# Performance work log

Measured on AMD Instinct MI355X. Metric: run time of the kernel, lower is better.

Reference implementation:

```python
import jax, jax.numpy as jnp
import numpy as np

S, D, H, E = 4096, 1024, 16, 64  # seq_len, embed_dim, n_heads, head_size


def setup_inputs() -> dict:
    key = jax.random.key(0)
    ks = jax.random.split(key, 8)
    s_d = 1.0 / np.sqrt(D).astype(np.float32)
    return {
        "x": jax.random.normal(ks[0], (S, D), jnp.float32),
        # per-head Q/K/V projections (no bias), stacked over heads: [H, D, E]
        "Wk": jax.random.normal(ks[1], (H, D, E), jnp.float32) * s_d,
        "Wq": jax.random.normal(ks[2], (H, D, E), jnp.float32) * s_d,
        "Wv": jax.random.normal(ks[3], (H, D, E), jnp.float32) * s_d,
        # output projection Dense(D) with bias
        "Wo": jax.random.normal(ks[4], (H * E, D), jnp.float32) * (1.0 / np.sqrt(H * E).astype(np.float32)),
        "bo": jnp.zeros((D,), jnp.float32),
        # MLP: Dense(4D) -> gelu -> Dense(D), both with bias
        "W1": jax.random.normal(ks[5], (D, 4 * D), jnp.float32) * s_d,
        "b1": jnp.zeros((4 * D,), jnp.float32),
        "W2": jax.random.normal(ks[6], (4 * D, D), jnp.float32) * (1.0 / np.sqrt(4 * D).astype(np.float32)),
        "b2": jnp.zeros((D,), jnp.float32),
    }


def _attention(x, Wk, Wq, Wv):
    # per-head projections, vectorized over heads (original loops in Python)
    k = jnp.einsum('sd,hde->hse', x, Wk)
    q = jnp.einsum('sd,hde->hse', x, Wq)
    v = jnp.einsum('sd,hde->hse', x, Wv)
    # NOTE: original computes keys @ queries.T -> scores[i, j] = k_i . q_j
    scores = jnp.einsum('hse,hte->hst', k, q) / jnp.sqrt(jnp.float32(E))
    mask = jnp.tril(jnp.ones((x.shape[0], x.shape[0]), dtype=bool))  # [S, S]
    w = jax.nn.softmax(jnp.where(mask, scores, -jnp.inf), axis=-1)   # [H, S, S]
    out = jnp.einsum('hst,hte->hse', w, v)                            # [H, S, E]
    # concatenate heads along feature axis (head 0 first, matching the loop)
    return out.transpose(1, 0, 2).reshape(x.shape[0], -1)             # [S, H*E]


def reference(x, Wk, Wq, Wv, Wo, bo, W1, b1, W2, b2):
    x = x + _attention(x, Wk, Wq, Wv) @ Wo + bo
    h = jax.nn.gelu(x @ W1 + b1, approximate=True)  # flax default gelu (tanh approx)
    return x + h @ W2 + b2
```

## Files before the change

### kernel.cpp

```cpp
#include <hip/hip_runtime.h>

typedef __attribute__((ext_vector_type(8))) short s16x8;
typedef __attribute__((ext_vector_type(4))) short s16x4;
typedef __attribute__((ext_vector_type(4))) float f32x4;


__device__ __forceinline__ unsigned short f2bf(float f) {
    union { float f; unsigned u; } v; v.f = f;
    unsigned r = v.u + 0x7FFFu + ((v.u >> 16) & 1u);
    return (unsigned short)(r >> 16);
}

__device__ __forceinline__ float bf2f(unsigned short b) {
    union { unsigned u; float f; } v; v.u = ((unsigned)b) << 16;
    return v.f;
}

__device__ __forceinline__ unsigned cvt_pk_bf16(float lo, float hi) {
    unsigned r;
    asm("v_cvt_pk_bf16_f32 %0, %1, %2" : "=v"(r) : "v"(lo), "v"(hi));
    return r;
}

__device__ __forceinline__ float exp2_fast(float x) {
    float r;
    asm("v_exp_f32 %0, %1" : "=v"(r) : "v"(x));
    return r;
}

__device__ __forceinline__ float gelu_tanh(float x) {
    float u = 0.7978845608028654f * (x + 0.044715f * x * x * x);
    float au = fabsf(u);
    float t = 1.f - 2.f / (__expf(2.f * au) + 1.f);
    t = (u < 0.f) ? -t : t;
    return 0.5f * x * (1.f + t);
}

__device__ __forceinline__ void load_lds16(const void* g, void* l) {
    __builtin_amdgcn_global_load_lds(
        (const __attribute__((address_space(1))) void*)g,
        (__attribute__((address_space(3))) void*)l, 16, 0, 0);
}

__device__ __forceinline__ void xcd_remap(int& bx, int& by) {
    const int gx = gridDim.x;
    const int nwg = gx * gridDim.y;
    const int id = by * gx + bx;
    const int nid = (id & 7) * (nwg >> 3) + (id >> 3);
    bx = nid % gx; by = nid / gx;
}


__global__ void convert_bf16_k(const float* __restrict__ in,
                               unsigned short* __restrict__ out, int n) {
    int i = (blockIdx.x * blockDim.x + threadIdx.x) * 4;
    if (i >= n) return;
    float4 v = *(const float4*)(in + i);
    ushort4 o;
    o.x = f2bf(v.x); o.y = f2bf(v.y); o.z = f2bf(v.z); o.w = f2bf(v.w);
    *(ushort4*)(out + i) = o;
}

__global__ void transpose_k(const float* __restrict__ in,
                            unsigned short* __restrict__ out, int R, int C) {
    __shared__ float tile[32][33];
    const int b = blockIdx.z;
    const int c0 = blockIdx.x * 32, r0 = blockIdx.y * 32;
    const float* inb = in + (size_t)b * R * C;
    unsigned short* outb = out + (size_t)b * R * C;
    const int tx = threadIdx.x, ty = threadIdx.y;
    #pragma unroll
    for (int i = 0; i < 4; ++i)
        tile[ty + i*8][tx] = inb[(size_t)(r0 + ty + i*8) * C + c0 + tx];
    __syncthreads();
    #pragma unroll
    for (int i = 0; i < 4; ++i)
        outb[(size_t)(c0 + ty + i*8) * R + r0 + tx] = f2bf(tile[tx][ty + i*8]);
}

template<int EPI>
__global__ __launch_bounds__(256) void gemm_bt(
    const unsigned short* __restrict__ A,
    const unsigned short* __restrict__ BT,
    const float* __restrict__ bias,
    const float* __restrict__ resid,
    float* __restrict__ Cf,
    unsigned short* __restrict__ Cb,
    int M, int N, int K, int klen)
{
    __shared__ unsigned short As[3][128 * 32];
    __shared__ unsigned short Bs[3][128 * 32];
    const int tid = threadIdx.x;
    const int w  = tid >> 6, l = tid & 63;
    const int wr = w >> 1,  wc = w & 1;
    const int lg = l >> 4,  ll = l & 15;
    int bx = blockIdx.x, by = blockIdx.y;
    xcd_remap(bx, by);
    const int m0 = by * 128, n0 = bx * 128;
    const int koff = (EPI == 5) ? (int)blockIdx.z * klen : 0;

    const int srow = w * 16 + (l >> 2);
    const int scol = (((l & 3) ^ ((l >> 2) & 3))) * 8;

    f32x4 acc[4][4] = {};

    auto stage = [&](int buf, int k0) {
        #pragma unroll
        for (int i = 0; i < 2; ++i) {
            load_lds16(A  + (size_t)(m0 + srow + i*64) * K + koff + k0 + scol,
                       (char*)As[buf] + i*4096 + w*1024);
            load_lds16(BT + (size_t)(n0 + srow + i*64) * K + koff + k0 + scol,
                       (char*)Bs[buf] + i*4096 + w*1024);
        }
    };

    const int nsteps = ((EPI == 5) ? klen : K) >> 5;
    stage(0, 0); stage(1, 32);
    int buf = 0;
    for (int s = 0; s < nsteps; ++s) {
        if (s + 1 < nsteps) asm volatile("s_waitcnt vmcnt(4)" ::: "memory");
        else                asm volatile("s_waitcnt vmcnt(0)" ::: "memory");
        __builtin_amdgcn_s_barrier();
        s16x8 a[4], b[4];
        #pragma unroll
        for (int m = 0; m < 4; ++m) {
            const int row = wr*64 + m*16 + ll;
            a[m] = *(const s16x8*)&As[buf][row * 32 + ((lg ^ (ll & 3)) * 8)];
        }
        #pragma unroll
        for (int n = 0; n < 4; ++n) {
            const int row = wc*64 + n*16 + ll;
            b[n] = *(const s16x8*)&Bs[buf][row * 32 + ((lg ^ (ll & 3)) * 8)];
        }
        int bnext = buf + 2; if (bnext >= 3) bnext -= 3;
        if (s + 2 < nsteps) stage(bnext, (s + 2) << 5);
        __builtin_amdgcn_s_setprio(1);
        #pragma unroll
        for (int m = 0; m < 4; ++m)
            #pragma unroll
            for (int n = 0; n < 4; ++n)
                acc[m][n] = __builtin_amdgcn_mfma_f32_16x16x32_bf16(a[m], b[n], acc[m][n], 0, 0, 0);
        __builtin_amdgcn_s_setprio(0);
        buf = (buf == 2) ? 0 : buf + 1;
    }

    unsigned short* Cbz = (EPI == 5) ? (Cb + (size_t)blockIdx.z * M * N) : Cb;
    #pragma unroll
    for (int m = 0; m < 4; ++m) {
        #pragma unroll
        for (int n = 0; n < 4; ++n) {
            const int col = n0 + wc*64 + n*16 + ll;
            #pragma unroll
            for (int r = 0; r < 4; ++r) {
                const int row = m0 + wr*64 + m*16 + lg*4 + r;
                float v = acc[m][n][r];
                if constexpr (EPI == 2) v = gelu_tanh(v + bias[col]);
                if constexpr (EPI == 4) v *= (col < 1024) ? 0.1803368801f : 1.0f;
                Cbz[(size_t)row * N + col] = f2bf(v);
            }
        }
    }
}

__global__ __launch_bounds__(512) void gemm_mlp1_k(
    const unsigned short* __restrict__ A,
    const unsigned short* __restrict__ BT,
    const float* __restrict__ bias,
    unsigned short* __restrict__ Cb,
    int M, int N, int K)
{
    __shared__ unsigned short As[3][256 * 32];
    __shared__ unsigned short Bs[3][128 * 32];
    const int tid = threadIdx.x;
    const int w  = tid >> 6, l = tid & 63;
    const int wr = w >> 1,  wc = w & 1;
    const int lg = l >> 4,  ll = l & 15;
    int bx = blockIdx.x, by = blockIdx.y;
    xcd_remap(bx, by);
    const int m0 = by * 256, n0 = bx * 128;

    const int srowA = w * 16 + (l >> 2);
    const int scolA = (((l & 3) ^ ((l >> 2) & 3))) * 8;
    const int srowB = tid >> 2;
    const int scolB = (((tid & 3) ^ ((tid >> 2) & 3))) * 8;

    f32x4 acc[4][4] = {};

    auto stage = [&](int buf, int k0) {
        #pragma unroll
        for (int i = 0; i < 2; ++i)
            load_lds16(A + (size_t)(m0 + srowA + i*128) * K + k0 + scolA,
                       (char*)As[buf] + i*8192 + w*1024);
        load_lds16(BT + (size_t)(n0 + srowB) * K + k0 + scolB,
                   (char*)Bs[buf] + w*1024);
    };

    const int nsteps = K >> 5;
    stage(0, 0); stage(1, 32);
    int buf = 0;
    for (int s = 0; s < nsteps; ++s) {
        if (s + 1 < nsteps) asm volatile("s_waitcnt vmcnt(3)" ::: "memory");
        else                asm volatile("s_waitcnt vmcnt(0)" ::: "memory");
        __builtin_amdgcn_s_barrier();
        s16x8 a[4], b[4];
        #pragma unroll
        for (int m = 0; m < 4; ++m) {
            const int row = wr*64 + m*16 + ll;
            a[m] = *(const s16x8*)&As[buf][row * 32 + ((lg ^ (ll & 3)) * 8)];
        }
        #pragma unroll
        for (int n = 0; n < 4; ++n) {
            const int row = wc*64 + n*16 + ll;
            b[n] = *(const s16x8*)&Bs[buf][row * 32 + ((lg ^ (ll & 3)) * 8)];
        }
        int bnext = buf + 2; if (bnext >= 3) bnext -= 3;
        if (s + 2 < nsteps) stage(bnext, (s + 2) << 5);
        __builtin_amdgcn_s_setprio(1);
        #pragma unroll
        for (int m = 0; m < 4; ++m)
            #pragma unroll
            for (int n = 0; n < 4; ++n)
                acc[m][n] = __builtin_amdgcn_mfma_f32_16x16x32_bf16(a[m], b[n], acc[m][n], 0, 0, 0);
        __builtin_amdgcn_s_setprio(0);
        buf = (buf == 2) ? 0 : buf + 1;
    }

    #pragma unroll
    for (int m = 0; m < 4; ++m) {
        #pragma unroll
        for (int n = 0; n < 4; ++n) {
            const int col = n0 + wc*64 + n*16 + ll;
            #pragma unroll
            for (int r = 0; r < 4; ++r) {
                const int row = m0 + wr*64 + m*16 + lg*4 + r;
                Cb[(size_t)row * N + col] = f2bf(gelu_tanh(acc[m][n][r] + bias[col]));
            }
        }
    }
}

template<int EPI>
__global__ __launch_bounds__(256) void gemm_bt64(
    const unsigned short* __restrict__ A,
    const unsigned short* __restrict__ BT,
    const float* __restrict__ bias,
    const float* __restrict__ resid,
    float* __restrict__ Cf,
    unsigned short* __restrict__ Cb,
    int M, int N, int K)
{
    __shared__ unsigned short As[4][128 * 32];
    __shared__ unsigned short Bs[4][64 * 32];
    const int tid = threadIdx.x;
    const int w  = tid >> 6, l = tid & 63;
    const int lg = l >> 4,  ll = l & 15;
    int bx = blockIdx.x, by = blockIdx.y;
    xcd_remap(bx, by);
    const int m0 = by * 128, n0 = bx * 64;

    const int srowA = w * 16 + (l >> 2);
    const int scolA = (((l & 3) ^ ((l >> 2) & 3))) * 8;
    const int srowB = tid >> 2;
    const int scolB = (((tid & 3) ^ ((tid >> 2) & 3))) * 8;

    f32x4 acc[2][4] = {};

    auto stage = [&](int buf, int k0) {
        #pragma unroll
        for (int i = 0; i < 2; ++i)
            load_lds16(A + (size_t)(m0 + srowA + i*64) * K + k0 + scolA,
                       (char*)As[buf] + i*4096 + w*1024);
        load_lds16(BT + (size_t)(n0 + srowB) * K + k0 + scolB,
                   (char*)Bs[buf] + w*1024);
    };

    const int nsteps = K >> 5;
    stage(0, 0); stage(1, 32); stage(2, 64);
    int buf = 0;
    for (int s = 0; s < nsteps; ++s) {
        const int rem = nsteps - 1 - s;
        if (rem >= 2)      asm volatile("s_waitcnt vmcnt(6)" ::: "memory");
        else if (rem == 1) asm volatile("s_waitcnt vmcnt(3)" ::: "memory");
        else               asm volatile("s_waitcnt vmcnt(0)" ::: "memory");
        __builtin_amdgcn_s_barrier();
        s16x8 a[2], b[4];
        #pragma unroll
        for (int m = 0; m < 2; ++m) {
            const int row = w*32 + m*16 + ll;
            a[m] = *(const s16x8*)&As[buf][row * 32 + ((lg ^ (ll & 3)) * 8)];
        }
        #pragma unroll
        for (int n = 0; n < 4; ++n) {
            const int row = n*16 + ll;
            b[n] = *(const s16x8*)&Bs[buf][row * 32 + ((lg ^ (ll & 3)) * 8)];
        }
        int bnext = buf + 3; if (bnext >= 4) bnext -= 4;
        if (s + 3 < nsteps) stage(bnext, (s + 3) << 5);
        __builtin_amdgcn_s_setprio(1);
        #pragma unroll
        for (int m = 0; m < 2; ++m)
            #pragma unroll
            for (int n = 0; n < 4; ++n)
                acc[m][n] = __builtin_amdgcn_mfma_f32_16x16x32_bf16(a[m], b[n], acc[m][n], 0, 0, 0);
        __builtin_amdgcn_s_setprio(0);
        buf = (buf + 1) & 3;
    }

    #pragma unroll
    for (int m = 0; m < 2; ++m) {
        #pragma unroll
        for (int n = 0; n < 4; ++n) {
            const int col = n0 + n*16 + ll;
            #pragma unroll
            for (int r = 0; r < 4; ++r) {
                const int row = m0 + w*32 + m*16 + lg*4 + r;
                float v = acc[m][n][r];
                if constexpr (EPI == 1) v += bias[col] + resid[(size_t)row * N + col];
                Cb[(size_t)row * N + col] = f2bf(v);
                if constexpr (EPI == 1)
                    Cf[(size_t)row * N + col] = v;
            }
        }
    }
}

__global__ __launch_bounds__(256) void mlp2_combine_k(
    const unsigned short* __restrict__ P,
    const float* __restrict__ bias,
    const float* __restrict__ resid,
    float* __restrict__ out)
{
    const int idx = (blockIdx.x * 256 + threadIdx.x) * 4;
    const int col = idx & 1023;
    ushort4 a = *(const ushort4*)(P + idx);
    ushort4 b = *(const ushort4*)(P + 4194304 + idx);
    float4 rs = *(const float4*)(resid + idx);
    float4 o;
    o.x = bf2f(a.x) + bf2f(b.x) + bias[col]     + rs.x;
    o.y = bf2f(a.y) + bf2f(b.y) + bias[col + 1] + rs.y;
    o.z = bf2f(a.z) + bf2f(b.z) + bias[col + 2] + rs.z;
    o.w = bf2f(a.w) + bf2f(b.w) + bias[col + 3] + rs.w;
    *(float4*)(out + idx) = o;
}

__global__ __launch_bounds__(512) void attn_k(
    const unsigned short* __restrict__ Rq,
    const unsigned short* __restrict__ Ck,
    const unsigned short* __restrict__ Vt,
    unsigned short* __restrict__ Ppart,
    float* __restrict__ Lpart)
{
    __shared__ unsigned short Ks[3][64 * 64];
    __shared__ unsigned short Vs[3][64 * 64];

    const int bx = blockIdx.x;
    const int h  = bx & 15;
    const int j  = (bx >> 4) & 1;
    const int sb = 15 - (bx >> 5);
    const int half = 2*sb + 2;
    const int t0 = j ? half : 0;
    const int t1 = j ? 2*half : half;

    const int tid = threadIdx.x;
    const int w = tid >> 6, l = tid & 63;
    const int lg = l >> 4, ll = l & 15;

    const int gsrc  = ((l & 7) ^ (l >> 3)) * 8;
    const int kOff  = (w*8 + (l >> 3)) * 2048 + h*64 + gsrc;
    const int vOff  = (h*64 + w*8 + (l >> 3)) * 4096 + gsrc;
    const int ldsOff = w * 1024;

    int qkoff[4][2];
    #pragma unroll
    for (int jj = 0; jj < 4; ++jj) {
        const int row = jj*16 + ll, r7 = row & 7;
        qkoff[jj][0] = row*128 + ((lg)     ^ r7) * 16;
        qkoff[jj][1] = row*128 + ((4 + lg) ^ r7) * 16;
    }
    int pvoff[4][2][2];
    #pragma unroll
    for (int n = 0; n < 4; ++n) {
        const int row = n*16 + ll, r7 = row & 7;
        #pragma unroll
        for (int c = 0; c < 2; ++c) {
            const int gl = (c*4     + (lg >> 1)) ^ r7;
            const int gh = (c*4 + 2 + (lg >> 1)) ^ r7;
            pvoff[n][c][0] = row*128 + gl*16 + (lg & 1)*8;
            pvoff[n][c][1] = row*128 + gh*16 + (lg & 1)*8;
        }
    }

    auto stage = [&](int t, int buf) {
        load_lds16(Ck + (size_t)t * 131072 + kOff, (char*)Ks[buf] + ldsOff);
        load_lds16(Vt + t * 64 + vOff,             (char*)Vs[buf] + ldsOff);
    };

    const int row0 = sb*256 + w*32;
    const int qgA  = row0 + ll;
    const int qgB  = row0 + 16 + ll;
    const size_t rbA = (size_t)qgA * 2048 + h*64;
    const size_t rbB = (size_t)qgB * 2048 + h*64;
    const s16x8 rA0 = *(const s16x8*)&Rq[rbA + lg*8];
    const s16x8 rA1 = *(const s16x8*)&Rq[rbA + 32 + lg*8];
    const s16x8 rB0 = *(const s16x8*)&Rq[rbB + lg*8];
    const s16x8 rB1 = *(const s16x8*)&Rq[rbB + 32 + lg*8];

    const short onebf = (short)0x3F80;
    const s16x8 ones = {onebf, onebf, onebf, onebf, onebf, onebf, onebf, onebf};

    f32x4 o[2][4] = {};
    f32x4 o4[2] = {};

    stage(t0, 0);
    stage(t0 + 1, 1);
    int buf = 0;

    for (int t = t0; t < t1; ++t) {
        if (t < t1-1) asm volatile("s_waitcnt vmcnt(2)" ::: "memory");
        else          asm volatile("s_waitcnt vmcnt(0)" ::: "memory");
        __builtin_amdgcn_s_barrier();
        const char* kb = (const char*)Ks[buf];
        const char* vb = (const char*)Vs[buf];
        const bool live = (t*64 <= row0 + 31);
        const bool anyMask = (t*64 + 63 > row0);

        f32x4 st[2][4];
        if (live) {
            __builtin_amdgcn_s_setprio(1);
            #pragma unroll
            for (int jj = 0; jj < 4; ++jj) {
                s16x8 k0 = *(const s16x8*)(kb + qkoff[jj][0]);
                s16x8 k1 = *(const s16x8*)(kb + qkoff[jj][1]);
                f32x4 z = {0.f, 0.f, 0.f, 0.f};
                f32x4 ta = __builtin_amdgcn_mfma_f32_16x16x32_bf16(k0, rA0, z, 0, 0, 0);
                st[0][jj] = __builtin_amdgcn_mfma_f32_16x16x32_bf16(k1, rA1, ta, 0, 0, 0);
                f32x4 tb = __builtin_amdgcn_mfma_f32_16x16x32_bf16(k0, rB0, z, 0, 0, 0);
                st[1][jj] = __builtin_amdgcn_mfma_f32_16x16x32_bf16(k1, rB1, tb, 0, 0, 0);
            }
            __builtin_amdgcn_s_setprio(0);
        }

        int bnext = buf + 2; if (bnext >= 3) bnext -= 3;
        if (t + 2 < t1) stage(t + 2, bnext);

        if (live) {
            float p[2][4][4];
            if (anyMask) {
                #pragma unroll
                for (int jj = 0; jj < 4; ++jj)
                    #pragma unroll
                    for (int r = 0; r < 4; ++r) {
                        const int jg = t*64 + jj*16 + lg*4 + r;
                        p[0][jj][r] = exp2_fast((jg > qgA) ? -3e38f : st[0][jj][r]);
                        p[1][jj][r] = exp2_fast((jg > qgB) ? -3e38f : st[1][jj][r]);
                    }
            } else {
                #pragma unroll
                for (int rs = 0; rs < 2; ++rs)
                    #pragma unroll
                    for (int jj = 0; jj < 4; ++jj)
                        #pragma unroll
                        for (int r = 0; r < 4; ++r)
                            p[rs][jj][r] = exp2_fast(st[rs][jj][r]);
            }

            s16x8 apv[2][2];
            #pragma unroll
            for (int rs = 0; rs < 2; ++rs)
                #pragma unroll
                for (int c = 0; c < 2; ++c) {
                    union { unsigned u[4]; s16x8 v; } pk;
                    pk.u[0] = cvt_pk_bf16(p[rs][2*c][0],   p[rs][2*c][1]);
                    pk.u[1] = cvt_pk_bf16(p[rs][2*c][2],   p[rs][2*c][3]);
                    pk.u[2] = cvt_pk_bf16(p[rs][2*c+1][0], p[rs][2*c+1][1]);
                    pk.u[3] = cvt_pk_bf16(p[rs][2*c+1][2], p[rs][2*c+1][3]);
                    apv[rs][c] = pk.v;
                }
            __builtin_amdgcn_s_setprio(1);
            #pragma unroll
            for (int rs = 0; rs < 2; ++rs) {
                o4[rs] = __builtin_amdgcn_mfma_f32_16x16x32_bf16(apv[rs][0], ones, o4[rs], 0, 0, 0);
                o4[rs] = __builtin_amdgcn_mfma_f32_16x16x32_bf16(apv[rs][1], ones, o4[rs], 0, 0, 0);
            }
            #pragma unroll
            for (int n = 0; n < 4; ++n) {
                #pragma unroll
                for (int c = 0; c < 2; ++c) {
                    s16x4 lo = *(const s16x4*)(vb + pvoff[n][c][0]);
                    s16x4 hi = *(const s16x4*)(vb + pvoff[n][c][1]);
                    union { s16x4 h2[2]; s16x8 v; } u;
                    u.h2[0] = lo; u.h2[1] = hi;
                    o[0][n] = __builtin_amdgcn_mfma_f32_16x16x32_bf16(apv[0][c], u.v, o[0][n], 0, 0, 0);
                    o[1][n] = __builtin_amdgcn_mfma_f32_16x16x32_bf16(apv[1][c], u.v, o[1][n], 0, 0, 0);
                }
            }
            __builtin_amdgcn_s_setprio(0);
        }

        buf = (buf == 2) ? 0 : buf + 1;
    }

    unsigned short* Pout = Ppart + (size_t)j * 4194304;
    float* Lout = Lpart + (size_t)j * 65536;
    #pragma unroll
    for (int rs = 0; rs < 2; ++rs)
        #pragma unroll
        for (int r = 0; r < 4; ++r) {
            const int row = row0 + rs*16 + lg*4 + r;
            const size_t orow = (size_t)row * 1024 + h * 64;
            #pragma unroll
            for (int n = 0; n < 4; ++n)
                Pout[orow + n*16 + ll] = f2bf(o[rs][n][r]);
            if (ll == 0) Lout[row * 16 + h] = o4[rs][r];
        }
}

__global__ __launch_bounds__(256) void attn_combine_k(
    const unsigned short* __restrict__ P,
    const float* __restrict__ L,
    unsigned short* __restrict__ Out)
{
    const int idx = (blockIdx.x * 256 + threadIdx.x) * 4;
    const int row = idx >> 10, h = (idx & 1023) >> 6;
    const float inv = 1.f / (L[row*16 + h] + L[65536 + row*16 + h]);
    ushort4 a = *(const ushort4*)(P + idx);
    ushort4 b = *(const ushort4*)(P + 4194304 + idx);
    ushort4 o;
    o.x = f2bf((bf2f(a.x) + bf2f(b.x)) * inv);
    o.y = f2bf((bf2f(a.y) + bf2f(b.y)) * inv);
    o.z = f2bf((bf2f(a.z) + bf2f(b.z)) * inv);
    o.w = f2bf((bf2f(a.w) + bf2f(b.w)) * inv);
    *(ushort4*)(Out + idx) = o;
}


extern "C" void kernel_launch(void* const* d_in, const int* in_sizes, int n_in,
                              void* d_out, int out_size, void* d_ws, size_t ws_size,
                              hipStream_t stream) {
    const float* x  = (const float*)d_in[0];
    const float* Wk = (const float*)d_in[1];
    const float* Wq = (const float*)d_in[2];
    const float* Wv = (const float*)d_in[3];
    const float* Wo = (const float*)d_in[4];
    const float* bo = (const float*)d_in[5];
    const float* W1 = (const float*)d_in[6];
    const float* b1 = (const float*)d_in[7];
    const float* W2 = (const float*)d_in[8];
    const float* b2 = (const float*)d_in[9];
    float* out = (float*)d_out;

    char* ws = (char*)d_ws;
    unsigned short* x_bf  = (unsigned short*)(ws);
    unsigned short* WqkT  = (unsigned short*)(ws + (8u  << 20));
    unsigned short* WvT   = (unsigned short*)(ws + (12u << 20));
    unsigned short* WoT   = (unsigned short*)(ws + (14u << 20));
    unsigned short* W1T   = (unsigned short*)(ws + (16u << 20));
    unsigned short* W2T   = (unsigned short*)(ws + (24u << 20));
    unsigned short* QKm   = (unsigned short*)(ws + (32u << 20));
    unsigned short* attn  = (unsigned short*)(ws + (48u << 20));
    unsigned short* Vt    = (unsigned short*)(ws + (56u << 20));
    float*          yf    = (float*)(ws + (64u << 20));
    float*          Lpart = (float*)ws;
    unsigned short* Ppart = (unsigned short*)(ws + (64u << 20));
    unsigned short* Pmlp  = (unsigned short*)(ws);
    unsigned short* y_bf  = x_bf;
    unsigned short* h_bf  = QKm;

    dim3 tb(32, 8);
    convert_bf16_k<<<4096, 256, 0, stream>>>(x, x_bf, 4096 * 1024);
    transpose_k<<<dim3(2, 32, 16),  tb, 0, stream>>>(Wq, WqkT,               1024, 64);
    transpose_k<<<dim3(2, 32, 16),  tb, 0, stream>>>(Wk, WqkT + 1024 * 1024, 1024, 64);
    transpose_k<<<dim3(2, 32, 16),  tb, 0, stream>>>(Wv, WvT, 1024, 64);
    transpose_k<<<dim3(32, 32, 1),  tb, 0, stream>>>(Wo, WoT, 1024, 1024);
    transpose_k<<<dim3(128, 32, 1), tb, 0, stream>>>(W1, W1T, 1024, 4096);
    transpose_k<<<dim3(32, 128, 1), tb, 0, stream>>>(W2, W2T, 4096, 1024);

    gemm_bt<4><<<dim3(16, 32), 256, 0, stream>>>(x_bf, WqkT, nullptr, nullptr, nullptr,
                                                 QKm, 4096, 2048, 1024, 1024);
    gemm_bt64<0><<<dim3(64, 8), 256, 0, stream>>>(WvT, x_bf, nullptr, nullptr, nullptr,
                                                  Vt, 1024, 4096, 1024);

    attn_k<<<512, 512, 0, stream>>>(QKm + 1024 , QKm , Vt, Ppart, Lpart);
    attn_combine_k<<<4096, 256, 0, stream>>>(Ppart, Lpart, attn);

    gemm_bt64<1><<<dim3(16, 32), 256, 0, stream>>>(attn, WoT, bo, x, yf, y_bf,
                                                   4096, 1024, 1024);
    gemm_mlp1_k<<<dim3(32, 16), 512, 0, stream>>>(y_bf, W1T, b1, h_bf, 4096, 4096, 1024);
    gemm_bt<5><<<dim3(8, 32, 2), 256, 0, stream>>>(h_bf, W2T, nullptr, nullptr, nullptr,
                                                   Pmlp, 4096, 1024, 4096, 2048);
    mlp2_combine_k<<<4096, 256, 0, stream>>>(Pmlp, b2, yf, out);
}
```

Measured before the change: 240.9 us.

## Pipeline attention K/V tiles in pairs and merge QKV weight transposes

The attention kernel moves from a 3-buffer ring that prefetches one tile ahead to 4 LDS buffers filled two tiles at a time. This halves the number of waitcnt/barrier points per tile, and the next pair's loads are issued before computing the current pair. The three separate Q/K/V weight transpose launches become one launch indexed by blockIdx.z. LDS use rises from 48KB to 64KB per block, and vmcnt(0) now waits for the whole prefetched pair, which may reduce overlap.

```diff
diff --git a/kernel.cpp b/kernel.cpp
--- a/kernel.cpp
+++ b/kernel.cpp
@@ -65,6 +65,30 @@
                             unsigned short* __restrict__ out, int R, int C) {
     __shared__ float tile[32][33];
     const int b = blockIdx.z;
+    const int c0 = blockIdx.x * 32, r0 = blockIdx.y * 32;
+    const float* inb = in + (size_t)b * R * C;
+    unsigned short* outb = out + (size_t)b * R * C;
+    const int tx = threadIdx.x, ty = threadIdx.y;
+    #pragma unroll
+    for (int i = 0; i < 4; ++i)
+        tile[ty + i*8][tx] = inb[(size_t)(r0 + ty + i*8) * C + c0 + tx];
+    __syncthreads();
+    #pragma unroll
+    for (int i = 0; i < 4; ++i)
+        outb[(size_t)(c0 + ty + i*8) * R + r0 + tx] = f2bf(tile[tx][ty + i*8]);
+}
+
+__global__ void transpose_qkv_k(const float* __restrict__ Wq,
+                                const float* __restrict__ Wk,
+                                const float* __restrict__ Wv,
+                                unsigned short* __restrict__ WqkT,
+                                unsigned short* __restrict__ WvT) {
+    __shared__ float tile[32][33];
+    const int z = blockIdx.z;
+    const int which = z >> 4, b = z & 15;
+    const float* in = (which == 0) ? Wq : (which == 1) ? Wk : Wv;
+    unsigned short* out = (which == 0) ? WqkT : (which == 1) ? (WqkT + 1024*1024) : WvT;
+    const int R = 1024, C = 64;
     const int c0 = blockIdx.x * 32, r0 = blockIdx.y * 32;
     const float* inb = in + (size_t)b * R * C;
     unsigned short* outb = out + (size_t)b * R * C;
@@ -154,7 +178,6 @@
             for (int r = 0; r < 4; ++r) {
                 const int row = m0 + wr*64 + m*16 + lg*4 + r;
                 float v = acc[m][n][r];
-                if constexpr (EPI == 2) v = gelu_tanh(v + bias[col]);
                 if constexpr (EPI == 4) v *= (col < 1024) ? 0.1803368801f : 1.0f;
                 Cbz[(size_t)row * N + col] = f2bf(v);
             }
@@ -350,8 +373,8 @@
     unsigned short* __restrict__ Ppart,
     float* __restrict__ Lpart)
 {
-    __shared__ unsigned short Ks[3][64 * 64];
-    __shared__ unsigned short Vs[3][64 * 64];
+    __shared__ unsigned short Ks[4][64 * 64];
+    __shared__ unsigned short Vs[4][64 * 64];
 
     const int bx = blockIdx.x;
     const int h  = bx & 15;
@@ -359,7 +382,7 @@
     const int sb = 15 - (bx >> 5);
     const int half = 2*sb + 2;
     const int t0 = j ? half : 0;
-    const int t1 = j ? 2*half : half;
+    const int npairs = sb + 1;
 
     const int tid = threadIdx.x;
     const int w = tid >> 6, l = tid & 63;
@@ -393,6 +416,12 @@
     auto stage = [&](int t, int buf) {
         load_lds16(Ck + (size_t)t * 131072 + kOff, (char*)Ks[buf] + ldsOff);
         load_lds16(Vt + t * 64 + vOff,             (char*)Vs[buf] + ldsOff);
+    };
+    auto stagePair = [&](int p) {
+        const int base = (p & 1) * 2;
+        const int t = t0 + 2*p;
+        stage(t,     base);
+        stage(t + 1, base + 1);
     };
 
     const int row0 = sb*256 + w*32;
@@ -411,93 +440,87 @@
     f32x4 o[2][4] = {};
     f32x4 o4[2] = {};
 
-    stage(t0, 0);
-    stage(t0 + 1, 1);
-    int buf = 0;
-
-    for (int t = t0; t < t1; ++t) {
-        if (t < t1-1) asm volatile("s_waitcnt vmcnt(2)" ::: "memory");
-        else          asm volatile("s_waitcnt vmcnt(0)" ::: "memory");
-        __builtin_amdgcn_s_barrier();
-        const char* kb = (const char*)Ks[buf];
-        const char* vb = (const char*)Vs[buf];
+    auto tileCompute = [&](int t, const char* kb, const char* vb) {
         const bool live = (t*64 <= row0 + 31);
         const bool anyMask = (t*64 + 63 > row0);
+        if (!live) return;
 
         f32x4 st[2][4];
-        if (live) {
-            __builtin_amdgcn_s_setprio(1);
-            #pragma unroll
-            for (int jj = 0; jj < 4; ++jj) {
-                s16x8 k0 = *(const s16x8*)(kb + qkoff[jj][0]);
-                s16x8 k1 = *(const s16x8*)(kb + qkoff[jj][1]);
-                f32x4 z = {0.f, 0.f, 0.f, 0.f};
-                f32x4 ta = __builtin_amdgcn_mfma_f32_16x16x32_bf16(k0, rA0, z, 0, 0, 0);
-                st[0][jj] = __builtin_amdgcn_mfma_f32_16x16x32_bf16(k1, rA1, ta, 0, 0, 0);
-                f32x4 tb = __builtin_amdgcn_mfma_f32_16x16x32_bf16(k0, rB0, z, 0, 0, 0);
-                st[1][jj] = __builtin_amdgcn_mfma_f32_16x16x32_bf16(k1, rB1, tb, 0, 0, 0);
-            }
-            __builtin_amdgcn_s_setprio(0);
-        }
-
-        int bnext = buf + 2; if (bnext >= 3) bnext -= 3;
-        if (t + 2 < t1) stage(t + 2, bnext);
-
-        if (live) {
-            float p[2][4][4];
-            if (anyMask) {
+        __builtin_amdgcn_s_setprio(1);
+        #pragma unroll
+        for (int jj = 0; jj < 4; ++jj) {
+            s16x8 k0 = *(const s16x8*)(kb + qkoff[jj][0]);
+            s16x8 k1 = *(const s16x8*)(kb + qkoff[jj][1]);
+            f32x4 z = {0.f, 0.f, 0.f, 0.f};
+            f32x4 ta = __builtin_amdgcn_mfma_f32_16x16x32_bf16(k0, rA0, z, 0, 0, 0);
+            st[0][jj] = __builtin_amdgcn_mfma_f32_16x16x32_bf16(k1, rA1, ta, 0, 0, 0);
+            f32x4 tb = __builtin_amdgcn_mfma_f32_16x16x32_bf16(k0, rB0, z, 0, 0, 0);
+            st[1][jj] = __builtin_amdgcn_mfma_f32_16x16x32_bf16(k1, rB1, tb, 0, 0, 0);
+        }
+        __builtin_amdgcn_s_setprio(0);
+
+        float p[2][4][4];
+        if (anyMask) {
+            #pragma unroll
+            for (int jj = 0; jj < 4; ++jj)
+                #pragma unroll
+                for (int r = 0; r < 4; ++r) {
+                    const int jg = t*64 + jj*16 + lg*4 + r;
+                    p[0][jj][r] = exp2_fast((jg > qgA) ? -3e38f : st[0][jj][r]);
+                    p[1][jj][r] = exp2_fast((jg > qgB) ? -3e38f : st[1][jj][r]);
+                }
+        } else {
+            #pragma unroll
+            for (int rs = 0; rs < 2; ++rs)
                 #pragma unroll
                 for (int jj = 0; jj < 4; ++jj)
                     #pragma unroll
-                    for (int r = 0; r < 4; ++r) {
-                        const int jg = t*64 + jj*16 + lg*4 + r;
-                        p[0][jj][r] = exp2_fast((jg > qgA) ? -3e38f : st[0][jj][r]);
-                        p[1][jj][r] = exp2_fast((jg > qgB) ? -3e38f : st[1][jj][r]);
-                    }
-            } else {
-                #pragma unroll
-                for (int rs = 0; rs < 2; ++rs)
-                    #pragma unroll
-                    for (int jj = 0; jj < 4; ++jj)
-                        #pragma unroll
-                        for (int r = 0; r < 4; ++r)
-                            p[rs][jj][r] = exp2_fast(st[rs][jj][r]);
+                    for (int r = 0; r < 4; ++r)
+                        p[rs][jj][r] = exp2_fast(st[rs][jj][r]);
+        }
+
+        s16x8 apv[2][2];
+        #pragma unroll
+        for (int rs = 0; rs < 2; ++rs)
+            #pragma unroll
+            for (int c = 0; c < 2; ++c) {
+                union { unsigned u[4]; s16x8 v; } pk;
+                pk.u[0] = cvt_pk_bf16(p[rs][2*c][0],   p[rs][2*c][1]);
+                pk.u[1] = cvt_pk_bf16(p[rs][2*c][2],   p[rs][2*c][3]);
+                pk.u[2] = cvt_pk_bf16(p[rs][2*c+1][0], p[rs][2*c+1][1]);
+                pk.u[3] = cvt_pk_bf16(p[rs][2*c+1][2], p[rs][2*c+1][3]);
+                apv[rs][c] = pk.v;
             }
-
-            s16x8 apv[2][2];
-            #pragma unroll
-            for (int rs = 0; rs < 2; ++rs)
-                #pragma unroll
-                for (int c = 0; c < 2; ++c) {
-                    union { unsigned u[4]; s16x8 v; } pk;
-                    pk.u[0] = cvt_pk_bf16(p[rs][2*c][0],   p[rs][2*c][1]);
-                    pk.u[1] = cvt_pk_bf16(p[rs][2*c][2],   p[rs][2*c][3]);
-                    pk.u[2] = cvt_pk_bf16(p[rs][2*c+1][0], p[rs][2*c+1][1]);
-                    pk.u[3] = cvt_pk_bf16(p[rs][2*c+1][2], p[rs][2*c+1][3]);
-                    apv[rs][c] = pk.v;
-                }
-            __builtin_amdgcn_s_setprio(1);
-            #pragma unroll
-            for (int rs = 0; rs < 2; ++rs) {
-                o4[rs] = __builtin_amdgcn_mfma_f32_16x16x32_bf16(apv[rs][0], ones, o4[rs], 0, 0, 0);
-                o4[rs] = __builtin_amdgcn_mfma_f32_16x16x32_bf16(apv[rs][1], ones, o4[rs], 0, 0, 0);
+        __builtin_amdgcn_s_setprio(1);
+        #pragma unroll
+        for (int rs = 0; rs < 2; ++rs) {
+            o4[rs] = __builtin_amdgcn_mfma_f32_16x16x32_bf16(apv[rs][0], ones, o4[rs], 0, 0, 0);
+            o4[rs] = __builtin_amdgcn_mfma_f32_16x16x32_bf16(apv[rs][1], ones, o4[rs], 0, 0, 0);
+        }
+        #pragma unroll
+        for (int n = 0; n < 4; ++n) {
+            #pragma unroll
+            for (int c = 0; c < 2; ++c) {
+                s16x4 lo = *(const s16x4*)(vb + pvoff[n][c][0]);
+                s16x4 hi = *(const s16x4*)(vb + pvoff[n][c][1]);
+                union { s16x4 h2[2]; s16x8 v; } u;
+                u.h2[0] = lo; u.h2[1] = hi;
+                o[0][n] = __builtin_amdgcn_mfma_f32_16x16x32_bf16(apv[0][c], u.v, o[0][n], 0, 0, 0);
+                o[1][n] = __builtin_amdgcn_mfma_f32_16x16x32_bf16(apv[1][c], u.v, o[1][n], 0, 0, 0);
             }
-            #pragma unroll
-            for (int n = 0; n < 4; ++n) {
-                #pragma unroll
-                for (int c = 0; c < 2; ++c) {
-                    s16x4 lo = *(const s16x4*)(vb + pvoff[n][c][0]);
-                    s16x4 hi = *(const s16x4*)(vb + pvoff[n][c][1]);
-                    union { s16x4 h2[2]; s16x8 v; } u;
-                    u.h2[0] = lo; u.h2[1] = hi;
-                    o[0][n] = __builtin_amdgcn_mfma_f32_16x16x32_bf16(apv[0][c], u.v, o[0][n], 0, 0, 0);
-                    o[1][n] = __builtin_amdgcn_mfma_f32_16x16x32_bf16(apv[1][c], u.v, o[1][n], 0, 0, 0);
-                }
-            }
-            __builtin_amdgcn_s_setprio(0);
-        }
-
-        buf = (buf == 2) ? 0 : buf + 1;
+        }
+        __builtin_amdgcn_s_setprio(0);
+    };
+
+    stagePair(0);
+    for (int p = 0; p < npairs; ++p) {
+        asm volatile("s_waitcnt vmcnt(0)" ::: "memory");
+        __builtin_amdgcn_s_barrier();
+        if (p + 1 < npairs) stagePair(p + 1);
+        const int base = (p & 1) * 2;
+        const int t = t0 + 2*p;
+        tileCompute(t,     (const char*)Ks[base],     (const char*)Vs[base]);
+        tileCompute(t + 1, (const char*)Ks[base + 1], (const char*)Vs[base + 1]);
     }
 
     unsigned short* Pout = Ppart + (size_t)j * 4194304;
@@ -568,9 +591,7 @@
 
     dim3 tb(32, 8);
     convert_bf16_k<<<4096, 256, 0, stream>>>(x, x_bf, 4096 * 1024);
-    transpose_k<<<dim3(2, 32, 16),  tb, 0, stream>>>(Wq, WqkT,               1024, 64);
-    transpose_k<<<dim3(2, 32, 16),  tb, 0, stream>>>(Wk, WqkT + 1024 * 1024, 1024, 64);
-    transpose_k<<<dim3(2, 32, 16),  tb, 0, stream>>>(Wv, WvT, 1024, 64);
+    transpose_qkv_k<<<dim3(2, 32, 48), tb, 0, stream>>>(Wq, Wk, Wv, WqkT, WvT);
     transpose_k<<<dim3(32, 32, 1),  tb, 0, stream>>>(Wo, WoT, 1024, 1024);
     transpose_k<<<dim3(128, 32, 1), tb, 0, stream>>>(W1, W1T, 1024, 4096);
     transpose_k<<<dim3(32, 128, 1), tb, 0, stream>>>(W2, W2T, 4096, 1024);
```

New measurement: 237.0 us. Within noise of the previous version (-1.6%).
